# Kernel tuning notes

Hardware: AMD Instinct MI355X
Metric: run time of the kernel (lower is better)

The kernel has to match this reference:

```python
import jax, jax.numpy as jnp
import numpy as np

BATCH = 1_000_000
IN_DIM = 3
OUT_DIM = 64


def setup_inputs() -> dict:
    key = jax.random.key(0)
    ks = jax.random.split(key, 14)
    names = ["S", "X", "Uz", "Ug", "Ur", "Uh", "Wz", "Wg", "Wr", "Wh", "bz", "bg", "br", "bh"]
    shapes = {
        "S": (BATCH, OUT_DIM), "X": (BATCH, IN_DIM),
        "Uz": (IN_DIM, OUT_DIM), "Ug": (IN_DIM, OUT_DIM), "Ur": (IN_DIM, OUT_DIM), "Uh": (IN_DIM, OUT_DIM),
        "Wz": (OUT_DIM, OUT_DIM), "Wg": (OUT_DIM, OUT_DIM), "Wr": (OUT_DIM, OUT_DIM), "Wh": (OUT_DIM, OUT_DIM),
        "bz": (1, OUT_DIM), "bg": (1, OUT_DIM), "br": (1, OUT_DIM), "bh": (1, OUT_DIM),
    }
    scale = {"S": 1.0, "X": 1.0}
    return {n: (jax.random.normal(k, shapes[n], dtype=jnp.float32) * scale.get(n, 0.2))
            for n, k in zip(names, ks)}


def reference(S, X, Uz, Ug, Ur, Uh, Wz, Wg, Wr, Wh, bz, bg, br, bh):
    # Custom DGM LSTM-style gated layer (activation_1 = activation_2 = tanh).
    Z = jnp.tanh(X @ Uz + S @ Wz + bz)
    G = jnp.tanh(X @ Ug + S @ Wg + bg)
    R = jnp.tanh(X @ Ur + S @ Wr + br)
    H = jnp.tanh(X @ Uh + (S * R) @ Wh + bh)
    S_new = (1.0 - G) * H + Z * S
    return S_new
```

## Files before the change

### kernel.cpp

```cpp
#include <hip/hip_runtime.h>

#define NWT   62500
#define GRID  512
#define WPB   4
#define TOTW  (GRID * WPB)

typedef __attribute__((ext_vector_type(8))) short bf16x8;
typedef __attribute__((ext_vector_type(4))) float f32x4;

static __device__ __forceinline__ short f2b(float f) {
    __bf16 h = (__bf16)f;
    return __builtin_bit_cast(short, h);
}
static __device__ __forceinline__ unsigned pack2(float lo, float hi) {
    return ((unsigned)(unsigned short)f2b(lo)) |
           (((unsigned)(unsigned short)f2b(hi)) << 16);
}
static __device__ __forceinline__ float bflo(unsigned u) {
    return __builtin_bit_cast(float, u << 16);
}
static __device__ __forceinline__ float bfhi(unsigned u) {
    return __builtin_bit_cast(float, u & 0xffff0000u);
}
static __device__ __forceinline__ float tanh_fast(float x) {
    float e = __builtin_exp2f(x * 2.8853900817779268f);
    return 1.0f - 2.0f * __builtin_amdgcn_rcpf(e + 1.0f);
}

static __device__ __forceinline__ void gate_mm_reg(const bf16x8 (&wR)[2][4],
                                                   const char* lBg, const int (&baOff)[4],
                                                   bf16x8 aX, bf16x8 a0, bf16x8 a1,
                                                   f32x4 (&acc)[4])
{
    #pragma unroll
    for (int nt = 0; nt < 4; ++nt) {
        bf16x8 bx = *(const bf16x8*)(lBg + baOff[nt]);
        f32x4 z4 = {0.f, 0.f, 0.f, 0.f};
        acc[nt] = __builtin_amdgcn_mfma_f32_16x16x32_bf16(bx, aX, z4, 0, 0, 0);
    }
    #pragma unroll
    for (int ks = 0; ks < 2; ++ks) {
        bf16x8 a = ks ? a1 : a0;
        #pragma unroll
        for (int nt = 0; nt < 4; ++nt)
            acc[nt] = __builtin_amdgcn_mfma_f32_16x16x32_bf16(wR[ks][nt], a, acc[nt], 0, 0, 0);
    }
}

__global__ __launch_bounds__(256, 2)
void dgm_lstm_kernel(const float* __restrict__ S, const float* __restrict__ X,
                     const float* __restrict__ U0, const float* __restrict__ U1,
                     const float* __restrict__ U2, const float* __restrict__ U3,
                     const float* __restrict__ W0, const float* __restrict__ W1,
                     const float* __restrict__ W2, const float* __restrict__ W3,
                     const float* __restrict__ b0, const float* __restrict__ b1,
                     const float* __restrict__ b2, const float* __restrict__ b3,
                     float* __restrict__ Out)
{
    __shared__ __align__(16) unsigned short lWT[4][64][64];
    __shared__ __align__(16) unsigned short lBa[4][65][8];
    __shared__ __align__(16) float          lS[WPB][16][68];
    __shared__ __align__(16) unsigned short lR[WPB][2][16][64];

    const int tid = threadIdx.x;

    {
        const float* Ws[4] = {W0, W1, W2, W3};
        #pragma unroll
        for (int g = 0; g < 4; ++g) {
            #pragma unroll
            for (int it = 0; it < 8; ++it) {
                int p  = it * 256 + tid;
                int n  = p & 63;
                int k2 = (p >> 6) << 1;
                float w0 = Ws[g][k2 * 64 + n];
                float w1 = Ws[g][k2 * 64 + 64 + n];
                int byt = ((n << 7) + (k2 << 1)) ^ ((n & 7) << 4);
                *(unsigned*)((char*)(&lWT[0][0][0]) + (g << 13) + byt) = pack2(w0, w1);
            }
        }
        const float* Us[4] = {U0, U1, U2, U3};
        const float* bs[4] = {b0, b1, b2, b3};
        int g = tid >> 6, n = tid & 63;
        bf16x8 f = {};
        f[0] = f2b(Us[g][n]);       f[1] = f2b(Us[g][64 + n]);
        f[2] = f2b(Us[g][128 + n]); f[3] = f2b(bs[g][n]);
        *(bf16x8*)(&lBa[g][n][0]) = f;
        if (tid < 4) { bf16x8 z = {}; *(bf16x8*)(&lBa[tid][64][0]) = z; }
    }
    __syncthreads();

    const int l   = tid & 63;
    const int wv  = tid >> 6;
    const int l15 = l & 15;
    const int lg  = l >> 4;

    const char* lWb = (const char*)(&lWT[0][0][0]);
    const char* lBb = (const char*)(&lBa[0][0][0]);
    char*       lRw = (char*)(&lR[wv][0][0][0]);

    bf16x8 wReg[3][2][4];
    #pragma unroll
    for (int g = 0; g < 3; ++g)
        #pragma unroll
        for (int ks = 0; ks < 2; ++ks)
            #pragma unroll
            for (int nt = 0; nt < 4; ++nt) {
                int n = l15 + (nt << 4);
                int byt = ((n << 7) + (ks << 6) + (lg << 4)) ^ ((n & 7) << 4);
                wReg[g][ks][nt] = *(const bf16x8*)(lWb + (g << 13) + byt);
            }

    int baOff[4];
    #pragma unroll
    for (int nt = 0; nt < 4; ++nt)
        baOff[nt] = ((lg == 0) ? (l15 + (nt << 4)) : 64) << 4;
    int wOffH[2][4];
    #pragma unroll
    for (int ks = 0; ks < 2; ++ks)
        #pragma unroll
        for (int nt = 0; nt < 4; ++nt) {
            int n = l15 + (nt << 4);
            wOffH[ks][nt] = ((n << 7) + (ks << 6) + (lg << 4)) ^ ((n & 7) << 4);
        }
    int wrOff[4];
    #pragma unroll
    for (int nt = 0; nt < 4; ++nt)
        wrOff[nt] = ((l15 << 7) + (nt << 5) + (lg << 3)) ^ ((l15 & 7) << 4);
    int rdOff[2];
    #pragma unroll
    for (int ks = 0; ks < 2; ++ks)
        rdOff[ks] = ((l15 << 7) + (ks << 6) + (lg << 4)) ^ ((l15 & 7) << 4);

    const int gw = blockIdx.x * WPB + wv;
    const short one_bf = (short)0x3F80;

    float4 p0, p1, p2, p3;
    float  px0 = 0.f, px1 = 0.f, px2 = 0.f;
    {
        const float* Sr = S + (size_t)((gw << 4) + l15) * 64 + (lg << 3);
        p0 = *(const float4*)(Sr);      p1 = *(const float4*)(Sr + 4);
        p2 = *(const float4*)(Sr + 32); p3 = *(const float4*)(Sr + 36);
        if (lg == 0) {
            const float* Xr = X + (size_t)((gw << 4) + l15) * 3;
            px0 = Xr[0]; px1 = Xr[1]; px2 = Xr[2];
        }
    }

    f32x4  zsC[4];
    uint2  gqp[4];
    bf16x8 aXp = {};
    int    rowH = 0, parH = 0, par = 0;

    auto RZG = [&](int wt) {
        const int row0 = wt << 4;

        float* lSr = &lS[wv][l15][0];
        *(float4*)(lSr + (lg << 3))      = p0;
        *(float4*)(lSr + (lg << 3) + 4)  = p1;
        *(float4*)(lSr + (lg << 3) + 32) = p2;
        *(float4*)(lSr + (lg << 3) + 36) = p3;

        bf16x8 aS0, aS1, aX = {};
        aS0[0] = f2b(p0.x); aS0[1] = f2b(p0.y); aS0[2] = f2b(p0.z); aS0[3] = f2b(p0.w);
        aS0[4] = f2b(p1.x); aS0[5] = f2b(p1.y); aS0[6] = f2b(p1.z); aS0[7] = f2b(p1.w);
        aS1[0] = f2b(p2.x); aS1[1] = f2b(p2.y); aS1[2] = f2b(p2.z); aS1[3] = f2b(p2.w);
        aS1[4] = f2b(p3.x); aS1[5] = f2b(p3.y); aS1[6] = f2b(p3.z); aS1[7] = f2b(p3.w);
        aX[0] = f2b(px0); aX[1] = f2b(px1); aX[2] = f2b(px2);
        aX[3] = (lg == 0) ? one_bf : (short)0;

        int tn = wt + TOTW;
        if (tn < NWT) {
            const float* Sr = S + (size_t)((tn << 4) + l15) * 64 + (lg << 3);
            p0 = *(const float4*)(Sr);      p1 = *(const float4*)(Sr + 4);
            p2 = *(const float4*)(Sr + 32); p3 = *(const float4*)(Sr + 36);
            if (lg == 0) {
                const float* Xr = X + (size_t)((tn << 4) + l15) * 3;
                px0 = Xr[0]; px1 = Xr[1]; px2 = Xr[2];
            }
        }

        asm volatile("s_waitcnt lgkmcnt(0)" ::: "memory");
        f32x4 sv[4];
        #pragma unroll
        for (int nt = 0; nt < 4; ++nt)
            sv[nt] = *(const f32x4*)(&lS[wv][l15][(nt << 4) + (lg << 2)]);

        f32x4 acc[4];

        char* lRp = lRw + (par << 11);
        gate_mm_reg(wReg[2], lBb + 2 * 1040, baOff, aX, aS0, aS1, acc);
        #pragma unroll
        for (int nt = 0; nt < 4; ++nt) {
            float sr0 = sv[nt][0] * tanh_fast(acc[nt][0]);
            float sr1 = sv[nt][1] * tanh_fast(acc[nt][1]);
            float sr2 = sv[nt][2] * tanh_fast(acc[nt][2]);
            float sr3 = sv[nt][3] * tanh_fast(acc[nt][3]);
            uint2 w;
            w.x = pack2(sr0, sr1);
            w.y = pack2(sr2, sr3);
            *(uint2*)(lRp + wrOff[nt]) = w;
        }

        gate_mm_reg(wReg[0], lBb, baOff, aX, aS0, aS1, acc);
        #pragma unroll
        for (int nt = 0; nt < 4; ++nt)
            #pragma unroll
            for (int j = 0; j < 4; ++j)
                zsC[nt][j] = tanh_fast(acc[nt][j]) * sv[nt][j];

        gate_mm_reg(wReg[1], lBb + 1040, baOff, aX, aS0, aS1, acc);
        #pragma unroll
        for (int nt = 0; nt < 4; ++nt) {
            float g0 = 1.0f - tanh_fast(acc[nt][0]);
            float g1 = 1.0f - tanh_fast(acc[nt][1]);
            float g2 = 1.0f - tanh_fast(acc[nt][2]);
            float g3 = 1.0f - tanh_fast(acc[nt][3]);
            gqp[nt].x = pack2(g0, g1);
            gqp[nt].y = pack2(g2, g3);
        }

        aXp = aX; rowH = row0; parH = par; par ^= 1;
    };

    auto HCOMB = [&]() {
        const char* lRp = lRw + (parH << 11);
        bf16x8 aR0 = *(const bf16x8*)(lRp + rdOff[0]);
        bf16x8 aR1 = *(const bf16x8*)(lRp + rdOff[1]);
        f32x4 acc[4];
        #pragma unroll
        for (int nt = 0; nt < 4; ++nt) {
            bf16x8 bx = *(const bf16x8*)(lBb + 3 * 1040 + baOff[nt]);
            f32x4 z4 = {0.f, 0.f, 0.f, 0.f};
            acc[nt] = __builtin_amdgcn_mfma_f32_16x16x32_bf16(bx, aXp, z4, 0, 0, 0);
        }
        #pragma unroll
        for (int ks = 0; ks < 2; ++ks) {
            bf16x8 a = ks ? aR1 : aR0;
            #pragma unroll
            for (int nt = 0; nt < 4; ++nt) {
                bf16x8 bw = *(const bf16x8*)(lWb + (3 << 13) + wOffH[ks][nt]);
                acc[nt] = __builtin_amdgcn_mfma_f32_16x16x32_bf16(bw, a, acc[nt], 0, 0, 0);
            }
        }
        float* Or = Out + (size_t)(rowH + l15) * 64 + (lg << 2);
        #pragma unroll
        for (int nt = 0; nt < 4; ++nt) {
            float4 o;
            o.x = fmaf(bflo(gqp[nt].x), tanh_fast(acc[nt][0]), zsC[nt][0]);
            o.y = fmaf(bfhi(gqp[nt].x), tanh_fast(acc[nt][1]), zsC[nt][1]);
            o.z = fmaf(bflo(gqp[nt].y), tanh_fast(acc[nt][2]), zsC[nt][2]);
            o.w = fmaf(bfhi(gqp[nt].y), tanh_fast(acc[nt][3]), zsC[nt][3]);
            *(float4*)(Or + (nt << 4)) = o;
        }
    };

    RZG(gw);
    for (int wt = gw + TOTW; wt < NWT; wt += TOTW) {
        HCOMB();
        RZG(wt);
    }
    HCOMB();
}

extern "C" void kernel_launch(void* const* d_in, const int* in_sizes, int n_in,
                              void* d_out, int out_size, void* d_ws, size_t ws_size,
                              hipStream_t stream) {
    dim3 grid(GRID), block(256);
    dgm_lstm_kernel<<<grid, block, 0, stream>>>(
        (const float*)d_in[0],  (const float*)d_in[1],
        (const float*)d_in[2],  (const float*)d_in[3],
        (const float*)d_in[4],  (const float*)d_in[5],
        (const float*)d_in[6],  (const float*)d_in[7],
        (const float*)d_in[8],  (const float*)d_in[9],
        (const float*)d_in[10], (const float*)d_in[11],
        (const float*)d_in[12], (const float*)d_in[13],
        (float*)d_out);
}
```

Before: 139.5 us.

## Raise occupancy to three blocks per CU by overlaying shared memory and trimming register weights

Keeps only the Z and R weight fragments in registers and reads the G and H weights from LDS. This cuts VGPR pressure so launch bounds can request three blocks per CU, and the grid grows to 768 blocks. The Z and R weights are staged in the regions later reused for the S tile and the R buffer, with an extra barrier after the register loads, so the total LDS footprint shrinks. The aim is more waves in flight to hide global-memory latency on this streaming kernel. The cost is extra LDS reads on the G-gate path and more LDS bandwidth pressure. The tanh helper now uses __expf instead of exp2, and the zero bias row is dropped, relying on zero activations for the lanes that used it.

```diff
diff --git a/kernel.cpp b/kernel.cpp
--- a/kernel.cpp
+++ b/kernel.cpp
@@ -1,12 +1,20 @@
 #include <hip/hip_runtime.h>
 
 #define NWT   62500
-#define GRID  512
+#define GRID  768
 #define WPB   4
 #define TOTW  (GRID * WPB)
 
 typedef __attribute__((ext_vector_type(8))) short bf16x8;
 typedef __attribute__((ext_vector_type(4))) float f32x4;
+
+#define OFF_WG   0
+#define OFF_WH   8192
+#define OFF_BA   16384
+#define OFF_LS   20480
+#define OFF_LR   37888
+#define LS_WSTR  4352
+#define LS_RSTR  272
 
 static __device__ __forceinline__ short f2b(float f) {
     __bf16 h = (__bf16)f;
@@ -23,7 +31,7 @@
     return __builtin_bit_cast(float, u & 0xffff0000u);
 }
 static __device__ __forceinline__ float tanh_fast(float x) {
-    float e = __builtin_exp2f(x * 2.8853900817779268f);
+    float e = __expf(2.0f * x);
     return 1.0f - 2.0f * __builtin_amdgcn_rcpf(e + 1.0f);
 }
 
@@ -47,7 +55,29 @@
     }
 }
 
-__global__ __launch_bounds__(256, 2)
+static __device__ __forceinline__ void gate_mm_lds(const char* lWg, const int (&wOff)[2][4],
+                                                   const char* lBg, const int (&baOff)[4],
+                                                   bf16x8 aX, bf16x8 a0, bf16x8 a1,
+                                                   f32x4 (&acc)[4])
+{
+    #pragma unroll
+    for (int nt = 0; nt < 4; ++nt) {
+        bf16x8 bx = *(const bf16x8*)(lBg + baOff[nt]);
+        f32x4 z4 = {0.f, 0.f, 0.f, 0.f};
+        acc[nt] = __builtin_amdgcn_mfma_f32_16x16x32_bf16(bx, aX, z4, 0, 0, 0);
+    }
+    #pragma unroll
+    for (int ks = 0; ks < 2; ++ks) {
+        bf16x8 a = ks ? a1 : a0;
+        #pragma unroll
+        for (int nt = 0; nt < 4; ++nt) {
+            bf16x8 bw = *(const bf16x8*)(lWg + wOff[ks][nt]);
+            acc[nt] = __builtin_amdgcn_mfma_f32_16x16x32_bf16(bw, a, acc[nt], 0, 0, 0);
+        }
+    }
+}
+
+__global__ __launch_bounds__(256, 3)
 void dgm_lstm_kernel(const float* __restrict__ S, const float* __restrict__ X,
                      const float* __restrict__ U0, const float* __restrict__ U1,
                      const float* __restrict__ U2, const float* __restrict__ U3,
@@ -57,17 +87,16 @@
                      const float* __restrict__ b2, const float* __restrict__ b3,
                      float* __restrict__ Out)
 {
-    __shared__ __align__(16) unsigned short lWT[4][64][64];
-    __shared__ __align__(16) unsigned short lBa[4][65][8];
-    __shared__ __align__(16) float          lS[WPB][16][68];
-    __shared__ __align__(16) unsigned short lR[WPB][2][16][64];
+    __shared__ __align__(16) char sm[54272];
 
     const int tid = threadIdx.x;
 
     {
-        const float* Ws[4] = {W0, W1, W2, W3};
+        const float* Ws[4]  = {W0, W1, W2, W3};
+        const int    dst[4] = {OFF_LS, OFF_WG, OFF_LR, OFF_WH};
         #pragma unroll
         for (int g = 0; g < 4; ++g) {
+            char* d = sm + dst[g];
             #pragma unroll
             for (int it = 0; it < 8; ++it) {
                 int p  = it * 256 + tid;
@@ -76,7 +105,7 @@
                 float w0 = Ws[g][k2 * 64 + n];
                 float w1 = Ws[g][k2 * 64 + 64 + n];
                 int byt = ((n << 7) + (k2 << 1)) ^ ((n & 7) << 4);
-                *(unsigned*)((char*)(&lWT[0][0][0]) + (g << 13) + byt) = pack2(w0, w1);
+                *(unsigned*)(d + byt) = pack2(w0, w1);
             }
         }
         const float* Us[4] = {U0, U1, U2, U3};
@@ -85,8 +114,7 @@
         bf16x8 f = {};
         f[0] = f2b(Us[g][n]);       f[1] = f2b(Us[g][64 + n]);
         f[2] = f2b(Us[g][128 + n]); f[3] = f2b(bs[g][n]);
-        *(bf16x8*)(&lBa[g][n][0]) = f;
-        if (tid < 4) { bf16x8 z = {}; *(bf16x8*)(&lBa[tid][64][0]) = z; }
+        *(bf16x8*)(sm + OFF_BA + ((g << 6) + n) * 16) = f;
     }
     __syncthreads();
 
@@ -95,33 +123,17 @@
     const int l15 = l & 15;
     const int lg  = l >> 4;
 
-    const char* lWb = (const char*)(&lWT[0][0][0]);
-    const char* lBb = (const char*)(&lBa[0][0][0]);
-    char*       lRw = (char*)(&lR[wv][0][0][0]);
-
-    bf16x8 wReg[3][2][4];
-    #pragma unroll
-    for (int g = 0; g < 3; ++g)
-        #pragma unroll
-        for (int ks = 0; ks < 2; ++ks)
-            #pragma unroll
-            for (int nt = 0; nt < 4; ++nt) {
-                int n = l15 + (nt << 4);
-                int byt = ((n << 7) + (ks << 6) + (lg << 4)) ^ ((n & 7) << 4);
-                wReg[g][ks][nt] = *(const bf16x8*)(lWb + (g << 13) + byt);
-            }
-
     int baOff[4];
     #pragma unroll
     for (int nt = 0; nt < 4; ++nt)
-        baOff[nt] = ((lg == 0) ? (l15 + (nt << 4)) : 64) << 4;
-    int wOffH[2][4];
+        baOff[nt] = (l15 + (nt << 4)) << 4;
+    int wOff[2][4];
     #pragma unroll
     for (int ks = 0; ks < 2; ++ks)
         #pragma unroll
         for (int nt = 0; nt < 4; ++nt) {
             int n = l15 + (nt << 4);
-            wOffH[ks][nt] = ((n << 7) + (ks << 6) + (lg << 4)) ^ ((n & 7) << 4);
+            wOff[ks][nt] = ((n << 7) + (ks << 6) + (lg << 4)) ^ ((n & 7) << 4);
         }
     int wrOff[4];
     #pragma unroll
@@ -131,6 +143,22 @@
     #pragma unroll
     for (int ks = 0; ks < 2; ++ks)
         rdOff[ks] = ((l15 << 7) + (ks << 6) + (lg << 4)) ^ ((l15 & 7) << 4);
+
+    bf16x8 wZ[2][4], wR[2][4];
+    #pragma unroll
+    for (int ks = 0; ks < 2; ++ks)
+        #pragma unroll
+        for (int nt = 0; nt < 4; ++nt) {
+            wZ[ks][nt] = *(const bf16x8*)(sm + OFF_LS + wOff[ks][nt]);
+            wR[ks][nt] = *(const bf16x8*)(sm + OFF_LR + wOff[ks][nt]);
+        }
+    __syncthreads();
+
+    const char* lBb = sm + OFF_BA;
+    const char* lWg = sm + OFF_WG;
+    const char* lWh = sm + OFF_WH;
+    char*       lSw = sm + OFF_LS + wv * LS_WSTR;
+    char*       lRw = sm + OFF_LR + (wv << 12);
 
     const int gw = blockIdx.x * WPB + wv;
     const short one_bf = (short)0x3F80;
@@ -155,11 +183,11 @@
     auto RZG = [&](int wt) {
         const int row0 = wt << 4;
 
-        float* lSr = &lS[wv][l15][0];
-        *(float4*)(lSr + (lg << 3))      = p0;
-        *(float4*)(lSr + (lg << 3) + 4)  = p1;
-        *(float4*)(lSr + (lg << 3) + 32) = p2;
-        *(float4*)(lSr + (lg << 3) + 36) = p3;
+        char* lSr = lSw + l15 * LS_RSTR;
+        *(float4*)(lSr + (lg << 5))        = p0;
+        *(float4*)(lSr + (lg << 5) + 16)   = p1;
+        *(float4*)(lSr + (lg << 5) + 128)  = p2;
+        *(float4*)(lSr + (lg << 5) + 144)  = p3;
 
         bf16x8 aS0, aS1, aX = {};
         aS0[0] = f2b(p0.x); aS0[1] = f2b(p0.y); aS0[2] = f2b(p0.z); aS0[3] = f2b(p0.w);
@@ -184,12 +212,12 @@
         f32x4 sv[4];
         #pragma unroll
         for (int nt = 0; nt < 4; ++nt)
-            sv[nt] = *(const f32x4*)(&lS[wv][l15][(nt << 4) + (lg << 2)]);
+            sv[nt] = *(const f32x4*)(lSw + l15 * LS_RSTR + (((nt << 4) + (lg << 2)) << 2));
 
         f32x4 acc[4];
 
         char* lRp = lRw + (par << 11);
-        gate_mm_reg(wReg[2], lBb + 2 * 1040, baOff, aX, aS0, aS1, acc);
+        gate_mm_reg(wR, lBb + 2 * 1024, baOff, aX, aS0, aS1, acc);
         #pragma unroll
         for (int nt = 0; nt < 4; ++nt) {
             float sr0 = sv[nt][0] * tanh_fast(acc[nt][0]);
@@ -202,14 +230,14 @@
             *(uint2*)(lRp + wrOff[nt]) = w;
         }
 
-        gate_mm_reg(wReg[0], lBb, baOff, aX, aS0, aS1, acc);
+        gate_mm_reg(wZ, lBb, baOff, aX, aS0, aS1, acc);
         #pragma unroll
         for (int nt = 0; nt < 4; ++nt)
             #pragma unroll
             for (int j = 0; j < 4; ++j)
                 zsC[nt][j] = tanh_fast(acc[nt][j]) * sv[nt][j];
 
-        gate_mm_reg(wReg[1], lBb + 1040, baOff, aX, aS0, aS1, acc);
+        gate_mm_lds(lWg, wOff, lBb + 1024, baOff, aX, aS0, aS1, acc);
         #pragma unroll
         for (int nt = 0; nt < 4; ++nt) {
             float g0 = 1.0f - tanh_fast(acc[nt][0]);
@@ -228,21 +256,7 @@
         bf16x8 aR0 = *(const bf16x8*)(lRp + rdOff[0]);
         bf16x8 aR1 = *(const bf16x8*)(lRp + rdOff[1]);
         f32x4 acc[4];
-        #pragma unroll
-        for (int nt = 0; nt < 4; ++nt) {
-            bf16x8 bx = *(const bf16x8*)(lBb + 3 * 1040 + baOff[nt]);
-            f32x4 z4 = {0.f, 0.f, 0.f, 0.f};
-            acc[nt] = __builtin_amdgcn_mfma_f32_16x16x32_bf16(bx, aXp, z4, 0, 0, 0);
-        }
-        #pragma unroll
-        for (int ks = 0; ks < 2; ++ks) {
-            bf16x8 a = ks ? aR1 : aR0;
-            #pragma unroll
-            for (int nt = 0; nt < 4; ++nt) {
-                bf16x8 bw = *(const bf16x8*)(lWb + (3 << 13) + wOffH[ks][nt]);
-                acc[nt] = __builtin_amdgcn_mfma_f32_16x16x32_bf16(bw, a, acc[nt], 0, 0, 0);
-            }
-        }
+        gate_mm_lds(lWh, wOff, lBb + 3 * 1024, baOff, aXp, aR0, aR1, acc);
         float* Or = Out + (size_t)(rowH + l15) * 64 + (lg << 2);
         #pragma unroll
         for (int nt = 0; nt < 4; ++nt) {
```

After: 128.1 us. -8.2%, faster.
